# Kernel tuning notes

Hardware: AMD Instinct MI355X
Metric: run time of the kernel (lower is better)

## Reference

```python
import jax, jax.numpy as jnp
import numpy as np

L, D, H, F = 6, 768, 12, 3072   # layers, d_model, heads, mlp hidden
B, S = 2, 2048                   # batch, seq_len
DH = D // H                      # head dim
EPS = 1e-5


def _layer_norm(x, w, b):
    mu = jnp.mean(x, axis=-1, keepdims=True)
    var = jnp.mean(jnp.square(x - mu), axis=-1, keepdims=True)
    return (x - mu) * jax.lax.rsqrt(var + EPS) * w + b


def setup_inputs() -> dict:
    key = jax.random.key(0)
    ks = jax.random.split(key, 8)
    w = lambda k, shape: jax.random.normal(k, shape, dtype=jnp.float32) * 0.02
    return {
        "x": jax.random.normal(ks[0], (B, S, D), dtype=jnp.float32),
        # attention projections, stacked over layers; weights stored (d_in, d_out)
        "Wq": w(ks[1], (L, D, D)), "bq": jnp.zeros((L, D), jnp.float32),
        "Wk": w(ks[2], (L, D, D)), "bk": jnp.zeros((L, D), jnp.float32),
        "Wv": w(ks[3], (L, D, D)), "bv": jnp.zeros((L, D), jnp.float32),
        "Wo": w(ks[4], (L, D, D)), "bo": jnp.zeros((L, D), jnp.float32),
        "ln1_w": jnp.ones((L, D), jnp.float32), "ln1_b": jnp.zeros((L, D), jnp.float32),
        "W1": w(ks[5], (L, D, F)), "b1": jnp.zeros((L, F), jnp.float32),
        "W2": w(ks[6], (L, F, D)), "b2": jnp.zeros((L, D), jnp.float32),
        "ln2_w": jnp.ones((L, D), jnp.float32), "ln2_b": jnp.zeros((L, D), jnp.float32),
        "lnf_w": jnp.ones((D,), jnp.float32), "lnf_b": jnp.zeros((D,), jnp.float32),
    }


def reference(x, Wq, bq, Wk, bk, Wv, bv, Wo, bo, ln1_w, ln1_b,
              W1, b1, W2, b2, ln2_w, ln2_b, lnf_w, lnf_b):
    scale = DH ** (-0.5)
    for i in range(L):
        # pre-norm MSA block; NB: residual uses the normalized x, as in source
        xn = _layer_norm(x, ln1_w[i], ln1_b[i])
        q = (xn @ Wq[i] + bq[i]).reshape(B, S, H, DH).transpose(0, 2, 1, 3)
        k = (xn @ Wk[i] + bk[i]).reshape(B, S, H, DH).transpose(0, 2, 1, 3)
        v = (xn @ Wv[i] + bv[i]).reshape(B, S, H, DH).transpose(0, 2, 1, 3)
        att = jax.nn.softmax(scale * jnp.einsum('bhqd,bhkd->bhqk', q, k), axis=-1)
        out = jnp.einsum('bhqk,bhkd->bhqd', att, v)
        out = out.transpose(0, 2, 1, 3).reshape(B, S, D)
        x = xn + (out @ Wo[i] + bo[i])
        # pre-norm FFN block; residual uses the normalized x, as in source
        xn2 = _layer_norm(x, ln2_w[i], ln2_b[i])
        h = jax.nn.gelu(xn2 @ W1[i] + b1[i], approximate=False)
        x = xn2 + (h @ W2[i] + b2[i])
    return _layer_norm(x, lnf_w, lnf_b)
```

## Files before the change

### kernel.cpp

```cpp
#include <hip/hip_runtime.h>
#include <stdint.h>

typedef unsigned short u16;
typedef unsigned int   u32;

#define L_N  6
#define D_N  768
#define F_N  3072
#define H_N  12
#define B_N  2
#define S_N  2048
#define BS_N 4096
#define QKV_N 2304

using bf16x8 = __attribute__((ext_vector_type(8))) short;
using f32x4  = __attribute__((ext_vector_type(4))) float;

__device__ __forceinline__ u16 f2bf(float f) {
  u32 x = __builtin_bit_cast(u32, f);
  x += 0x7FFFu + ((x >> 16) & 1u);
  return (u16)(x >> 16);
}

__device__ __forceinline__ u32 cvt_pk_bf16(float lo, float hi) {
  u32 r;
  asm("v_cvt_pk_bf16_f32 %0, %1, %2" : "=v"(r) : "v"(lo), "v"(hi));
  return r;
}

#define GLOAD16(g, l)                                                                     \
  __builtin_amdgcn_global_load_lds((const __attribute__((address_space(1))) void*)(g),    \
                                   (__attribute__((address_space(3))) void*)(l), 16, 0, 0)

__global__ __launch_bounds__(256) void transpose_cast_kernel(
    const float* __restrict__ in, u16* __restrict__ out, int K, int N,
    size_t out_lstride, int out_rowoff)
{
  __shared__ float tile[32][33];
  const int l  = blockIdx.z;
  const int n0 = blockIdx.x * 32, k0 = blockIdx.y * 32;
  const int tx = threadIdx.x & 31, ty = threadIdx.x >> 5;
  const float* src = in + (size_t)l * K * N;
  u16* dst = out + (size_t)l * out_lstride + (size_t)out_rowoff * K;
#pragma unroll
  for (int i = 0; i < 4; ++i)
    tile[ty + i * 8][tx] = src[(size_t)(k0 + ty + i * 8) * N + n0 + tx];
  __syncthreads();
#pragma unroll
  for (int i = 0; i < 4; ++i)
    dst[(size_t)(n0 + ty + i * 8) * K + k0 + tx] = f2bf(tile[tx][ty + i * 8]);
}

__global__ __launch_bounds__(256) void concat_bias_kernel(
    const float* __restrict__ bq, const float* __restrict__ bk,
    const float* __restrict__ bv, float* __restrict__ out)
{
  const int i = blockIdx.x * 256 + threadIdx.x;
  const int l = i / QKV_N, c = i - l * QKV_N;
  float v = (c < 768) ? bq[l * 768 + c]
          : (c < 1536) ? bk[l * 768 + c - 768]
                       : bv[l * 768 + c - 1536];
  out[i] = v;
}

__global__ __launch_bounds__(256) void ln_kernel(
    const float* __restrict__ x, const float* __restrict__ w, const float* __restrict__ b,
    float* __restrict__ outF, u16* __restrict__ outB)
{
  const int row = blockIdx.x, tid = threadIdx.x;
  const float* xr = x + (size_t)row * D_N;
  float v[3];
  float s = 0.f;
#pragma unroll
  for (int i = 0; i < 3; ++i) { v[i] = xr[tid + i * 256]; s += v[i]; }
  __shared__ float red[8];
  const int wave = tid >> 6, lane = tid & 63;
#pragma unroll
  for (int o = 32; o > 0; o >>= 1) s += __shfl_down(s, o, 64);
  if (lane == 0) red[wave] = s;
  __syncthreads();
  const float mu = (red[0] + red[1] + red[2] + red[3]) * (1.f / D_N);
  float d2 = 0.f;
#pragma unroll
  for (int i = 0; i < 3; ++i) { float d = v[i] - mu; d2 += d * d; }
#pragma unroll
  for (int o = 32; o > 0; o >>= 1) d2 += __shfl_down(d2, o, 64);
  if (lane == 0) red[4 + wave] = d2;
  __syncthreads();
  const float var = (red[4] + red[5] + red[6] + red[7]) * (1.f / D_N);
  const float rs = rsqrtf(var + 1e-5f);
#pragma unroll
  for (int i = 0; i < 3; ++i) {
    const int c = tid + i * 256;
    const float o = (v[i] - mu) * rs * w[c] + b[c];
    if (outF) outF[(size_t)row * D_N + c] = o;
    if (outB) outB[(size_t)row * D_N + c] = f2bf(o);
  }
}

template<bool GELU, bool RES, bool OUTF, bool OUTB>
__global__ __launch_bounds__(256) void gemm_kernel(
    const u16* __restrict__ A, const u16* __restrict__ Wt,
    const float* __restrict__ bias, const float* __restrict__ resid,
    float* __restrict__ outF, u16* __restrict__ outB,
    int M, int N, int K)
{
  __shared__ __align__(16) u16 As[2][128 * 32];
  __shared__ __align__(16) u16 Bs[2][128 * 32];
  const int tid  = threadIdx.x;
  const int wave = tid >> 6, lane = tid & 63;
  const int lr = lane & 15, lg = lane >> 4;
  const int row0 = blockIdx.x * 128, col0 = blockIdx.y * 128;
  const int wr = (wave >> 1) * 64, wc = (wave & 1) * 64;

  const int cb0 = wave * 64;
  const int cb1 = 256 + wave * 64;
  const int r0s = (cb0 + lane) >> 2, c0s = ((cb0 + lane) & 3) << 3;
  const int r1s = (cb1 + lane) >> 2, c1s = ((cb1 + lane) & 3) << 3;

  f32x4 acc[4][4] = {};

#define STAGE(cbuf, kk)                                                           \
  do {                                                                            \
    GLOAD16(A  + (size_t)(row0 + r0s) * K + (kk) + c0s, &As[cbuf][cb0 * 8]);      \
    GLOAD16(Wt + (size_t)(col0 + r0s) * K + (kk) + c0s, &Bs[cbuf][cb0 * 8]);      \
    GLOAD16(A  + (size_t)(row0 + r1s) * K + (kk) + c1s, &As[cbuf][cb1 * 8]);      \
    GLOAD16(Wt + (size_t)(col0 + r1s) * K + (kk) + c1s, &Bs[cbuf][cb1 * 8]);      \
  } while (0)

  STAGE(0, 0);
  __syncthreads();

  int c = 0;
  for (int k0 = 0; k0 < K; k0 += 32, c ^= 1) {
    if (k0 + 32 < K) STAGE(c ^ 1, k0 + 32);
    bf16x8 af[4], bfr[4];
#pragma unroll
    for (int m = 0; m < 4; ++m)
      af[m] = *(const bf16x8*)&As[c][(wr + m * 16 + lr) * 32 + lg * 8];
#pragma unroll
    for (int n = 0; n < 4; ++n)
      bfr[n] = *(const bf16x8*)&Bs[c][(wc + n * 16 + lr) * 32 + lg * 8];
    __builtin_amdgcn_s_setprio(1);
#pragma unroll
    for (int m = 0; m < 4; ++m)
#pragma unroll
      for (int n = 0; n < 4; ++n)
        acc[m][n] = __builtin_amdgcn_mfma_f32_16x16x32_bf16(af[m], bfr[n], acc[m][n], 0, 0, 0);
    __builtin_amdgcn_s_setprio(0);
    __syncthreads();
  }
#undef STAGE

#pragma unroll
  for (int m = 0; m < 4; ++m)
#pragma unroll
    for (int n = 0; n < 4; ++n) {
      const int col = col0 + wc + n * 16 + lr;
      const float bv = bias[col];
#pragma unroll
      for (int r = 0; r < 4; ++r) {
        const int row = row0 + wr + m * 16 + lg * 4 + r;
        float v = acc[m][n][r] + bv;
        if (GELU) v = 0.5f * v * (1.f + erff(v * 0.70710678118f));
        const size_t idx = (size_t)row * N + col;
        if (RES)  v += resid[idx];
        if (OUTF) outF[idx] = v;
        if (OUTB) outB[idx] = f2bf(v);
      }
    }
}

__global__ __launch_bounds__(256) void gemm64_kernel(
    const u16* __restrict__ A, const u16* __restrict__ Wt,
    const float* __restrict__ bias, const float* __restrict__ resid,
    float* __restrict__ outF, int M, int N, int K)
{
  __shared__ __align__(16) u16 As[2][64 * 32];
  __shared__ __align__(16) u16 Bs[2][64 * 32];
  const int tid  = threadIdx.x;
  const int wave = tid >> 6, lane = tid & 63;
  const int lr = lane & 15, lg = lane >> 4;
  const int row0 = blockIdx.x * 64, col0 = blockIdx.y * 64;
  const int wr = (wave >> 1) * 32, wc = (wave & 1) * 32;

  const int cb = wave * 64;
  const int ch = cb + lane;
  const int rs = ch >> 2, cs = (ch & 3) << 3;

  f32x4 acc[2][2] = {};

#define STAGE64(cbuf, kk)                                                         \
  do {                                                                            \
    GLOAD16(A  + (size_t)(row0 + rs) * K + (kk) + cs, &As[cbuf][cb * 8]);         \
    GLOAD16(Wt + (size_t)(col0 + rs) * K + (kk) + cs, &Bs[cbuf][cb * 8]);         \
  } while (0)

  STAGE64(0, 0);
  __syncthreads();

  int c = 0;
  for (int k0 = 0; k0 < K; k0 += 32, c ^= 1) {
    if (k0 + 32 < K) STAGE64(c ^ 1, k0 + 32);
    bf16x8 af[2], bfr[2];
#pragma unroll
    for (int m = 0; m < 2; ++m)
      af[m] = *(const bf16x8*)&As[c][(wr + m * 16 + lr) * 32 + lg * 8];
#pragma unroll
    for (int n = 0; n < 2; ++n)
      bfr[n] = *(const bf16x8*)&Bs[c][(wc + n * 16 + lr) * 32 + lg * 8];
    __builtin_amdgcn_s_setprio(1);
#pragma unroll
    for (int m = 0; m < 2; ++m)
#pragma unroll
      for (int n = 0; n < 2; ++n)
        acc[m][n] = __builtin_amdgcn_mfma_f32_16x16x32_bf16(af[m], bfr[n], acc[m][n], 0, 0, 0);
    __builtin_amdgcn_s_setprio(0);
    __syncthreads();
  }
#undef STAGE64

#pragma unroll
  for (int m = 0; m < 2; ++m)
#pragma unroll
    for (int n = 0; n < 2; ++n) {
      const int col = col0 + wc + n * 16 + lr;
      const float bv = bias[col];
#pragma unroll
      for (int r = 0; r < 4; ++r) {
        const int row = row0 + wr + m * 16 + lg * 4 + r;
        const size_t idx = (size_t)row * N + col;
        outF[idx] = acc[m][n][r] + bv + resid[idx];
      }
    }
}

#define CSC  0.18033688011112042f
#define DTHR 11.54f
__global__ __launch_bounds__(256) void attn_kernel(
    const u16* __restrict__ QKV, float* __restrict__ Opart, float* __restrict__ Ml)
{
  constexpr int LDQ = QKV_N;
  constexpr int NT  = S_N / 64;
  __shared__ __align__(16) u16 Ks [64 * 72];
  __shared__ __align__(16) u16 VTs[64 * 72];
  __shared__ __align__(16) u16 Ps [64 * 72];
  const int tid  = threadIdx.x;
  const int wave = tid >> 6, lane = tid & 63;
  const int lr = lane & 15, lg = lane >> 4;
  const int bh = blockIdx.y;
  const int b = bh / H_N, h = bh - b * H_N;
  const int q0 = blockIdx.x * 64;
  const int z  = blockIdx.z;
  const size_t rowbase = (size_t)b * S_N * LDQ;
  const u16* Qg = QKV + rowbase + h * 64;
  const u16* Kg = QKV + rowbase + 768 + h * 64;
  const u16* Vg = QKV + rowbase + 1536 + h * 64;

  const int qrow = q0 + wave * 16 + lr;
  const bf16x8 qf0 = *(const bf16x8*)(Qg + (size_t)qrow * LDQ + lg * 8);
  const bf16x8 qf1 = *(const bf16x8*)(Qg + (size_t)qrow * LDQ + 32 + lg * 8);

  f32x4 o_acc[4] = {};
  float m = -1e30f, l = 0.f;

  const int kr = tid >> 2, kc = (tid & 3) * 16;
  const int pp = tid >> 3, cg = tid & 7;

  for (int t = z * (NT / 2); t < (z + 1) * (NT / 2); ++t) {
    __syncthreads();
    {
      const u16* g = Kg + (size_t)(t * 64 + kr) * LDQ + kc;
      *(uint4*)&Ks[kr * 72 + kc]     = *(const uint4*)g;
      *(uint4*)&Ks[kr * 72 + kc + 8] = *(const uint4*)(g + 8);
      const u16* gv = Vg + (size_t)(t * 64 + 2 * pp) * LDQ + cg * 8;
      uint4 v0 = *(const uint4*)gv;
      uint4 v1 = *(const uint4*)(gv + LDQ);
      const u16* a0 = (const u16*)&v0;
      const u16* a1 = (const u16*)&v1;
#pragma unroll
      for (int j = 0; j < 8; ++j) {
        const int jj = (j + cg) & 7;
        *(u32*)&VTs[(cg * 8 + jj) * 72 + 2 * pp] = (u32)a0[jj] | ((u32)a1[jj] << 16);
      }
    }
    __syncthreads();

    f32x4 sv[4];
    __builtin_amdgcn_s_setprio(1);
#pragma unroll
    for (int kt = 0; kt < 4; ++kt) {
      const bf16x8 k0 = *(const bf16x8*)&Ks[(kt * 16 + lr) * 72 + lg * 8];
      const bf16x8 k1 = *(const bf16x8*)&Ks[(kt * 16 + lr) * 72 + 32 + lg * 8];
      f32x4 z4 = {};
      z4 = __builtin_amdgcn_mfma_f32_16x16x32_bf16(k0, qf0, z4, 0, 0, 0);
      z4 = __builtin_amdgcn_mfma_f32_16x16x32_bf16(k1, qf1, z4, 0, 0, 0);
      sv[kt] = z4;
    }
    __builtin_amdgcn_s_setprio(0);

    float mx = sv[0][0];
#pragma unroll
    for (int kt = 0; kt < 4; ++kt)
#pragma unroll
      for (int r = 0; r < 4; ++r) mx = fmaxf(mx, sv[kt][r]);
    mx = fmaxf(mx, __shfl_xor(mx, 16, 64));
    mx = fmaxf(mx, __shfl_xor(mx, 32, 64));
    mx *= CSC;
    if (!__all(mx - m <= DTHR)) {
      const float mn = fmaxf(m, mx);
      const float al = __builtin_amdgcn_exp2f(m - mn);
      m = mn;
      l *= al;
#pragma unroll
      for (int dt = 0; dt < 4; ++dt)
#pragma unroll
        for (int r = 0; r < 4; ++r) o_acc[dt][r] *= al;
    }
    float rs = 0.f;
#pragma unroll
    for (int kt = 0; kt < 4; ++kt)
#pragma unroll
      for (int r = 0; r < 4; ++r) {
        const float e = __builtin_amdgcn_exp2f(sv[kt][r] * CSC - m);
        sv[kt][r] = e;
        rs += e;
      }
    rs += __shfl_xor(rs, 16, 64);
    rs += __shfl_xor(rs, 32, 64);
    l += rs;

    u16* prow = &Ps[(wave * 16 + lr) * 72];
#pragma unroll
    for (int kt = 0; kt < 4; ++kt) {
      *(u32*)(prow + kt * 16 + lg * 4)     = cvt_pk_bf16(sv[kt][0], sv[kt][1]);
      *(u32*)(prow + kt * 16 + lg * 4 + 2) = cvt_pk_bf16(sv[kt][2], sv[kt][3]);
    }
    const bf16x8 pa0 = *(const bf16x8*)(prow + lg * 8);
    const bf16x8 pa1 = *(const bf16x8*)(prow + 32 + lg * 8);
    __builtin_amdgcn_s_setprio(1);
#pragma unroll
    for (int dt = 0; dt < 4; ++dt) {
      const bf16x8 w0 = *(const bf16x8*)&VTs[(dt * 16 + lr) * 72 + lg * 8];
      const bf16x8 w1 = *(const bf16x8*)&VTs[(dt * 16 + lr) * 72 + 32 + lg * 8];
      o_acc[dt] = __builtin_amdgcn_mfma_f32_16x16x32_bf16(w0, pa0, o_acc[dt], 0, 0, 0);
      o_acc[dt] = __builtin_amdgcn_mfma_f32_16x16x32_bf16(w1, pa1, o_acc[dt], 0, 0, 0);
    }
    __builtin_amdgcn_s_setprio(0);
  }

  float* op = Opart + ((((size_t)z * B_N + b) * H_N + h) * S_N + qrow) * 64;
#pragma unroll
  for (int dt = 0; dt < 4; ++dt)
    *(f32x4*)(op + dt * 16 + lg * 4) = o_acc[dt];
  if (lg == 0) {
    float* mlp = Ml + ((((size_t)z * B_N + b) * H_N + h) * S_N + qrow) * 2;
    mlp[0] = m; mlp[1] = l;
  }
}

__global__ __launch_bounds__(256) void attn_combine_kernel(
    const float* __restrict__ Opart, const float* __restrict__ Ml, u16* __restrict__ O)
{
  constexpr size_t HALF = (size_t)B_N * H_N * S_N;
  const int tid = threadIdx.x;
  const int lane = tid & 63, grp = tid >> 6;
  const size_t row = (size_t)blockIdx.x * 4 + grp;
  const float* p0 = Opart + row * 64;
  const float* p1 = p0 + HALF * 64;
  const float m0 = Ml[row * 2], l0 = Ml[row * 2 + 1];
  const float m1 = Ml[(row + HALF) * 2], l1 = Ml[(row + HALF) * 2 + 1];
  const float mm = fmaxf(m0, m1);
  const float a0 = __builtin_amdgcn_exp2f(m0 - mm);
  const float a1 = __builtin_amdgcn_exp2f(m1 - mm);
  const float inv = 1.f / (a0 * l0 + a1 * l1);
  const float o = (a0 * p0[lane] + a1 * p1[lane]) * inv;
  const int bh = (int)(row / S_N), s = (int)(row % S_N);
  const int b = bh / H_N, h = bh - b * H_N;
  O[((size_t)b * S_N + s) * D_N + h * 64 + lane] = f2bf(o);
}

extern "C" void kernel_launch(void* const* d_in, const int* in_sizes, int n_in,
                              void* d_out, int out_size, void* d_ws, size_t ws_size,
                              hipStream_t stream)
{
  (void)in_sizes; (void)n_in; (void)out_size; (void)ws_size;
  const float* x0   = (const float*)d_in[0];
  const float* Wq   = (const float*)d_in[1];
  const float* bq   = (const float*)d_in[2];
  const float* Wk   = (const float*)d_in[3];
  const float* bk   = (const float*)d_in[4];
  const float* Wv   = (const float*)d_in[5];
  const float* bv   = (const float*)d_in[6];
  const float* Wo   = (const float*)d_in[7];
  const float* bo   = (const float*)d_in[8];
  const float* ln1w = (const float*)d_in[9];
  const float* ln1b = (const float*)d_in[10];
  const float* W1   = (const float*)d_in[11];
  const float* b1   = (const float*)d_in[12];
  const float* W2   = (const float*)d_in[13];
  const float* b2   = (const float*)d_in[14];
  const float* ln2w = (const float*)d_in[15];
  const float* ln2b = (const float*)d_in[16];
  const float* lnfw = (const float*)d_in[17];
  const float* lnfb = (const float*)d_in[18];

  char* ws = (char*)d_ws;
  size_t off = 0;
  auto alloc = [&](size_t bytes) {
    char* p = ws + off; off += (bytes + 255) & ~(size_t)255; return p;
  };
  u16*   wqkv_t = (u16*)alloc((size_t)L_N * QKV_N * D_N * 2);
  u16*   wo_t   = (u16*)alloc((size_t)L_N * D_N * D_N * 2);
  u16*   w1_t   = (u16*)alloc((size_t)L_N * D_N * F_N * 2);
  u16*   w2_t   = (u16*)alloc((size_t)L_N * D_N * F_N * 2);
  float* bqkv   = (float*)alloc((size_t)L_N * QKV_N * 4);
  float* x_f    = (float*)alloc((size_t)BS_N * D_N * 4);
  float* xn_f   = (float*)alloc((size_t)BS_N * D_N * 4);
  u16*   xn_b   = (u16*)alloc((size_t)BS_N * D_N * 2);
  u16*   qkvb   = (u16*)alloc((size_t)BS_N * QKV_N * 2);
  u16*   ab     = (u16*)alloc((size_t)BS_N * D_N * 2);
  u16*   hb     = (u16*)alloc((size_t)BS_N * F_N * 2);
  float* ml     = (float*)alloc((size_t)2 * B_N * H_N * S_N * 2 * 4);
  float* opart  = (float*)hb;

  const size_t dd = (size_t)D_N * D_N, qs = (size_t)QKV_N * D_N, df = (size_t)D_N * F_N;
  transpose_cast_kernel<<<dim3(D_N/32, D_N/32, L_N), 256, 0, stream>>>(Wq, wqkv_t, D_N, D_N, qs, 0);
  transpose_cast_kernel<<<dim3(D_N/32, D_N/32, L_N), 256, 0, stream>>>(Wk, wqkv_t, D_N, D_N, qs, 768);
  transpose_cast_kernel<<<dim3(D_N/32, D_N/32, L_N), 256, 0, stream>>>(Wv, wqkv_t, D_N, D_N, qs, 1536);
  transpose_cast_kernel<<<dim3(D_N/32, D_N/32, L_N), 256, 0, stream>>>(Wo, wo_t, D_N, D_N, dd, 0);
  transpose_cast_kernel<<<dim3(F_N/32, D_N/32, L_N), 256, 0, stream>>>(W1, w1_t, D_N, F_N, df, 0);
  transpose_cast_kernel<<<dim3(D_N/32, F_N/32, L_N), 256, 0, stream>>>(W2, w2_t, F_N, D_N, df, 0);
  concat_bias_kernel<<<(L_N * QKV_N) / 256, 256, 0, stream>>>(bq, bk, bv, bqkv);

  const dim3 gQKV(BS_N / 128, QKV_N / 128);
  const dim3 gF  (BS_N / 128, F_N / 128);
  const dim3 g64 (BS_N / 64,  D_N / 64);
  const dim3 gA  (S_N / 64, B_N * H_N, 2);

  const float* xin = x0;
  for (int i = 0; i < L_N; ++i) {
    ln_kernel<<<BS_N, 256, 0, stream>>>(xin, ln1w + i * D_N, ln1b + i * D_N, xn_f, xn_b);
    gemm_kernel<false,false,false,true><<<gQKV, 256, 0, stream>>>(
        xn_b, wqkv_t + (size_t)i * qs, bqkv + (size_t)i * QKV_N, nullptr,
        nullptr, qkvb, BS_N, QKV_N, D_N);
    attn_kernel<<<gA, 256, 0, stream>>>(qkvb, opart, ml);
    attn_combine_kernel<<<(B_N * H_N * S_N) / 4, 256, 0, stream>>>(opart, ml, ab);
    gemm64_kernel<<<g64, 256, 0, stream>>>(
        ab, wo_t + (size_t)i * dd, bo + i * D_N, xn_f, x_f, BS_N, D_N, D_N);
    ln_kernel<<<BS_N, 256, 0, stream>>>(x_f, ln2w + i * D_N, ln2b + i * D_N, xn_f, xn_b);
    gemm_kernel<true,false,false,true><<<gF, 256, 0, stream>>>(
        xn_b, w1_t + (size_t)i * df, b1 + i * F_N, nullptr, nullptr, hb, BS_N, F_N, D_N);
    gemm64_kernel<<<g64, 256, 0, stream>>>(
        hb, w2_t + (size_t)i * df, b2 + i * D_N, xn_f, x_f, BS_N, D_N, F_N);
    xin = x_f;
  }
  ln_kernel<<<BS_N, 256, 0, stream>>>(x_f, lnfw, lnfb, (float*)d_out, nullptr);
}
```

Baseline: 1.485 ms.

## Drop split-KV attention combine, fold Q scale into GEMM, add XCD swizzle

The attention kernel stops splitting the KV range into two halves and no longer needs the separate combine pass. It writes normalized bf16 output directly, which removes the fp32 partial-output and max/sum round trips through memory plus one kernel launch per layer. The softmax row sum is now computed on the MFMA unit by multiplying P with a row of ones, replacing shuffle reductions. The Q scale is folded into the QKV GEMM epilogue, and both GEMMs remap block IDs for XCD locality. Halving the attention grid to 768 blocks may reduce occupancy and latency hiding. Folding the scale before the bf16 rounding of Q slightly changes numerics.

```diff
diff --git a/kernel.cpp b/kernel.cpp
--- a/kernel.cpp
+++ b/kernel.cpp
@@ -12,6 +12,8 @@
 #define S_N  2048
 #define BS_N 4096
 #define QKV_N 2304
+#define CSC  0.18033688011112042f
+#define DTHR 11.54f
 
 using bf16x8 = __attribute__((ext_vector_type(8))) short;
 using f32x4  = __attribute__((ext_vector_type(4))) float;
@@ -26,6 +28,16 @@
   u32 r;
   asm("v_cvt_pk_bf16_f32 %0, %1, %2" : "=v"(r) : "v"(lo), "v"(hi));
   return r;
+}
+
+__device__ __forceinline__ void xcd_swizzle(int& bx, int& by) {
+  const int gx  = (int)gridDim.x;
+  const int nwg = gx * (int)gridDim.y;
+  const int bid = (int)blockIdx.y * gx + (int)blockIdx.x;
+  const int q = nwg >> 3, r = nwg & 7;
+  const int xcd = bid & 7, idx = bid >> 3;
+  const int wg = (xcd < r ? xcd * (q + 1) : r * (q + 1) + (xcd - r) * q) + idx;
+  bx = wg % gx; by = wg / gx;
 }
 
 #define GLOAD16(g, l)                                                                     \
@@ -98,7 +110,7 @@
   }
 }
 
-template<bool GELU, bool RES, bool OUTF, bool OUTB>
+template<bool GELU, bool RES, bool OUTF, bool OUTB, bool SCALEQ>
 __global__ __launch_bounds__(256) void gemm_kernel(
     const u16* __restrict__ A, const u16* __restrict__ Wt,
     const float* __restrict__ bias, const float* __restrict__ resid,
@@ -110,7 +122,9 @@
   const int tid  = threadIdx.x;
   const int wave = tid >> 6, lane = tid & 63;
   const int lr = lane & 15, lg = lane >> 4;
-  const int row0 = blockIdx.x * 128, col0 = blockIdx.y * 128;
+  int bx, by;
+  xcd_swizzle(bx, by);
+  const int row0 = bx * 128, col0 = by * 128;
   const int wr = (wave >> 1) * 64, wc = (wave & 1) * 64;
 
   const int cb0 = wave * 64;
@@ -163,6 +177,7 @@
         const int row = row0 + wr + m * 16 + lg * 4 + r;
         float v = acc[m][n][r] + bv;
         if (GELU) v = 0.5f * v * (1.f + erff(v * 0.70710678118f));
+        if (SCALEQ && col < 768) v *= CSC;
         const size_t idx = (size_t)row * N + col;
         if (RES)  v += resid[idx];
         if (OUTF) outF[idx] = v;
@@ -181,7 +196,9 @@
   const int tid  = threadIdx.x;
   const int wave = tid >> 6, lane = tid & 63;
   const int lr = lane & 15, lg = lane >> 4;
-  const int row0 = blockIdx.x * 64, col0 = blockIdx.y * 64;
+  int bx, by;
+  xcd_swizzle(bx, by);
+  const int row0 = bx * 64, col0 = by * 64;
   const int wr = (wave >> 1) * 32, wc = (wave & 1) * 32;
 
   const int cb = wave * 64;
@@ -235,15 +252,13 @@
     }
 }
 
-#define CSC  0.18033688011112042f
-#define DTHR 11.54f
 __global__ __launch_bounds__(256) void attn_kernel(
-    const u16* __restrict__ QKV, float* __restrict__ Opart, float* __restrict__ Ml)
+    const u16* __restrict__ QKV, u16* __restrict__ O)
 {
   constexpr int LDQ = QKV_N;
   constexpr int NT  = S_N / 64;
   __shared__ __align__(16) u16 Ks [64 * 72];
-  __shared__ __align__(16) u16 VTs[64 * 72];
+  __shared__ __align__(16) u16 VTs[80 * 72];
   __shared__ __align__(16) u16 Ps [64 * 72];
   const int tid  = threadIdx.x;
   const int wave = tid >> 6, lane = tid & 63;
@@ -251,23 +266,30 @@
   const int bh = blockIdx.y;
   const int b = bh / H_N, h = bh - b * H_N;
   const int q0 = blockIdx.x * 64;
-  const int z  = blockIdx.z;
   const size_t rowbase = (size_t)b * S_N * LDQ;
   const u16* Qg = QKV + rowbase + h * 64;
   const u16* Kg = QKV + rowbase + 768 + h * 64;
   const u16* Vg = QKV + rowbase + 1536 + h * 64;
 
+  for (int i = tid; i < 16 * 72; i += 256)
+    VTs[64 * 72 + i] = (i < 64) ? (u16)0x3F80 : (u16)0;
+
   const int qrow = q0 + wave * 16 + lr;
   const bf16x8 qf0 = *(const bf16x8*)(Qg + (size_t)qrow * LDQ + lg * 8);
   const bf16x8 qf1 = *(const bf16x8*)(Qg + (size_t)qrow * LDQ + 32 + lg * 8);
 
+  __syncthreads();
+  const bf16x8 la0 = *(const bf16x8*)&VTs[(64 + lr) * 72 + lg * 8];
+  const bf16x8 la1 = *(const bf16x8*)&VTs[(64 + lr) * 72 + 32 + lg * 8];
+
   f32x4 o_acc[4] = {};
-  float m = -1e30f, l = 0.f;
+  f32x4 l_acc = {};
+  float m = -1e30f;
 
   const int kr = tid >> 2, kc = (tid & 3) * 16;
   const int pp = tid >> 3, cg = tid & 7;
 
-  for (int t = z * (NT / 2); t < (z + 1) * (NT / 2); ++t) {
+  for (int t = 0; t < NT; ++t) {
     __syncthreads();
     {
       const u16* g = Kg + (size_t)(t * 64 + kr) * LDQ + kc;
@@ -306,29 +328,21 @@
       for (int r = 0; r < 4; ++r) mx = fmaxf(mx, sv[kt][r]);
     mx = fmaxf(mx, __shfl_xor(mx, 16, 64));
     mx = fmaxf(mx, __shfl_xor(mx, 32, 64));
-    mx *= CSC;
     if (!__all(mx - m <= DTHR)) {
       const float mn = fmaxf(m, mx);
       const float al = __builtin_amdgcn_exp2f(m - mn);
       m = mn;
-      l *= al;
+      l_acc[0] *= al;
 #pragma unroll
       for (int dt = 0; dt < 4; ++dt)
 #pragma unroll
         for (int r = 0; r < 4; ++r) o_acc[dt][r] *= al;
     }
-    float rs = 0.f;
 #pragma unroll
     for (int kt = 0; kt < 4; ++kt)
 #pragma unroll
-      for (int r = 0; r < 4; ++r) {
-        const float e = __builtin_amdgcn_exp2f(sv[kt][r] * CSC - m);
-        sv[kt][r] = e;
-        rs += e;
-      }
-    rs += __shfl_xor(rs, 16, 64);
-    rs += __shfl_xor(rs, 32, 64);
-    l += rs;
+      for (int r = 0; r < 4; ++r)
+        sv[kt][r] = __builtin_amdgcn_exp2f(sv[kt][r] - m);
 
     u16* prow = &Ps[(wave * 16 + lr) * 72];
 #pragma unroll
@@ -346,38 +360,19 @@
       o_acc[dt] = __builtin_amdgcn_mfma_f32_16x16x32_bf16(w0, pa0, o_acc[dt], 0, 0, 0);
       o_acc[dt] = __builtin_amdgcn_mfma_f32_16x16x32_bf16(w1, pa1, o_acc[dt], 0, 0, 0);
     }
+    l_acc = __builtin_amdgcn_mfma_f32_16x16x32_bf16(la0, pa0, l_acc, 0, 0, 0);
+    l_acc = __builtin_amdgcn_mfma_f32_16x16x32_bf16(la1, pa1, l_acc, 0, 0, 0);
     __builtin_amdgcn_s_setprio(0);
   }
 
-  float* op = Opart + ((((size_t)z * B_N + b) * H_N + h) * S_N + qrow) * 64;
-#pragma unroll
-  for (int dt = 0; dt < 4; ++dt)
-    *(f32x4*)(op + dt * 16 + lg * 4) = o_acc[dt];
-  if (lg == 0) {
-    float* mlp = Ml + ((((size_t)z * B_N + b) * H_N + h) * S_N + qrow) * 2;
-    mlp[0] = m; mlp[1] = l;
-  }
-}
-
-__global__ __launch_bounds__(256) void attn_combine_kernel(
-    const float* __restrict__ Opart, const float* __restrict__ Ml, u16* __restrict__ O)
-{
-  constexpr size_t HALF = (size_t)B_N * H_N * S_N;
-  const int tid = threadIdx.x;
-  const int lane = tid & 63, grp = tid >> 6;
-  const size_t row = (size_t)blockIdx.x * 4 + grp;
-  const float* p0 = Opart + row * 64;
-  const float* p1 = p0 + HALF * 64;
-  const float m0 = Ml[row * 2], l0 = Ml[row * 2 + 1];
-  const float m1 = Ml[(row + HALF) * 2], l1 = Ml[(row + HALF) * 2 + 1];
-  const float mm = fmaxf(m0, m1);
-  const float a0 = __builtin_amdgcn_exp2f(m0 - mm);
-  const float a1 = __builtin_amdgcn_exp2f(m1 - mm);
-  const float inv = 1.f / (a0 * l0 + a1 * l1);
-  const float o = (a0 * p0[lane] + a1 * p1[lane]) * inv;
-  const int bh = (int)(row / S_N), s = (int)(row % S_N);
-  const int b = bh / H_N, h = bh - b * H_N;
-  O[((size_t)b * S_N + s) * D_N + h * 64 + lane] = f2bf(o);
+  const float lv = __shfl(l_acc[0], lr, 64);
+  const float inv = 1.f / lv;
+  u16* orow = O + (size_t)(b * S_N + qrow) * D_N + h * 64;
+#pragma unroll
+  for (int dt = 0; dt < 4; ++dt) {
+    *(u32*)(orow + dt * 16 + lg * 4)     = cvt_pk_bf16(o_acc[dt][0] * inv, o_acc[dt][1] * inv);
+    *(u32*)(orow + dt * 16 + lg * 4 + 2) = cvt_pk_bf16(o_acc[dt][2] * inv, o_acc[dt][3] * inv);
+  }
 }
 
 extern "C" void kernel_launch(void* const* d_in, const int* in_sizes, int n_in,
@@ -421,8 +416,6 @@
   u16*   qkvb   = (u16*)alloc((size_t)BS_N * QKV_N * 2);
   u16*   ab     = (u16*)alloc((size_t)BS_N * D_N * 2);
   u16*   hb     = (u16*)alloc((size_t)BS_N * F_N * 2);
-  float* ml     = (float*)alloc((size_t)2 * B_N * H_N * S_N * 2 * 4);
-  float* opart  = (float*)hb;
 
   const size_t dd = (size_t)D_N * D_N, qs = (size_t)QKV_N * D_N, df = (size_t)D_N * F_N;
   transpose_cast_kernel<<<dim3(D_N/32, D_N/32, L_N), 256, 0, stream>>>(Wq, wqkv_t, D_N, D_N, qs, 0);
@@ -436,20 +429,19 @@
   const dim3 gQKV(BS_N / 128, QKV_N / 128);
   const dim3 gF  (BS_N / 128, F_N / 128);
   const dim3 g64 (BS_N / 64,  D_N / 64);
-  const dim3 gA  (S_N / 64, B_N * H_N, 2);
+  const dim3 gA  (S_N / 64, B_N * H_N);
 
   const float* xin = x0;
   for (int i = 0; i < L_N; ++i) {
     ln_kernel<<<BS_N, 256, 0, stream>>>(xin, ln1w + i * D_N, ln1b + i * D_N, xn_f, xn_b);
-    gemm_kernel<false,false,false,true><<<gQKV, 256, 0, stream>>>(
+    gemm_kernel<false,false,false,true,true><<<gQKV, 256, 0, stream>>>(
         xn_b, wqkv_t + (size_t)i * qs, bqkv + (size_t)i * QKV_N, nullptr,
         nullptr, qkvb, BS_N, QKV_N, D_N);
-    attn_kernel<<<gA, 256, 0, stream>>>(qkvb, opart, ml);
-    attn_combine_kernel<<<(B_N * H_N * S_N) / 4, 256, 0, stream>>>(opart, ml, ab);
+    attn_kernel<<<gA, 256, 0, stream>>>(qkvb, ab);
     gemm64_kernel<<<g64, 256, 0, stream>>>(
         ab, wo_t + (size_t)i * dd, bo + i * D_N, xn_f, x_f, BS_N, D_N, D_N);
     ln_kernel<<<BS_N, 256, 0, stream>>>(x_f, ln2w + i * D_N, ln2b + i * D_N, xn_f, xn_b);
-    gemm_kernel<true,false,false,true><<<gF, 256, 0, stream>>>(
+    gemm_kernel<true,false,false,true,false><<<gF, 256, 0, stream>>>(
         xn_b, w1_t + (size_t)i * df, b1 + i * F_N, nullptr, nullptr, hb, BS_N, F_N, D_N);
     gemm64_kernel<<<g64, 256, 0, stream>>>(
         hb, w2_t + (size_t)i * df, b2 + i * D_N, xn_f, x_f, BS_N, D_N, F_N);
```

Measured after the change: 1.602 ms. 7.9% more time.
